# Kernel tuning notes

Hardware: AMD Instinct MI355X
Metric: run time of the kernel (lower is better)

The kernel has to match this reference:

```python
import jax, jax.numpy as jnp
import numpy as np

B, S, D, DOUT, E = 2, 2048, 1024, 1024, 8
DH = 4 * D  # expert hidden size


def setup_inputs() -> dict:
    key = jax.random.key(0)
    ks = jax.random.split(key, 7)
    sc = lambda *sh: 1.0 / np.sqrt(sh[-2]) if len(sh) >= 2 else 0.02
    return {
        "x": jax.random.normal(ks[0], (B, S, D), jnp.float32),
        "Wg": jax.random.normal(ks[1], (D, E), jnp.float32) / np.sqrt(D),
        "bg": jnp.zeros((E,), jnp.float32),
        "W1": jax.random.normal(ks[2], (E, D, DH), jnp.float32) / np.sqrt(D),
        "b1": jax.random.normal(ks[3], (E, DH), jnp.float32) * 0.02,
        "W2": jax.random.normal(ks[4], (E, DH, DOUT), jnp.float32) / np.sqrt(DH),
        "b2": jax.random.normal(ks[5], (E, DOUT), jnp.float32) * 0.02,
    }


def reference(x, Wg, bg, W1, b1, W2, b2):
    # x: [B, S, D] -> flatten tokens (chunking over seq in the original is
    # math-neutral: routing and expert MLP are per-token).
    Bb, Ss, Dd = x.shape
    xt = x.reshape(-1, Dd)                       # [T, D]
    # Gate: softmax then argmax (top-1 routing, output NOT scaled by gate prob)
    gates = jax.nn.softmax(xt @ Wg + bg, axis=-1)  # [T, E]
    sel = jnp.argmax(gates, axis=-1)               # [T]
    nE = W1.shape[0]
    out = jnp.zeros((xt.shape[0], W2.shape[-1]), x.dtype)
    # Grouped expert MLP expressed as masked dense loop over the small fixed
    # expert count (jit-friendly; a fused gather-grouped-GEMM-scatter kernel
    # is the optimization target).
    for e in range(nE):
        h = jax.nn.gelu(xt @ W1[e] + b1[e], approximate=False)  # [T, 4D]
        ye = h @ W2[e] + b2[e]                                  # [T, DOUT]
        out = jnp.where((sel == e)[:, None], ye, out)
    return out.reshape(Bb, Ss, -1)
```

## Files before the change

kernel.cpp:

```cpp
#include <hip/hip_runtime.h>
#include <hip/hip_bf16.h>
#include <math.h>

#define T_TOK 4096
#define DIM   1024
#define NEXP  8
#define DHID  4096
#define NDOUT 1024
#define BM    128
#define BN    128
#define BK    64
#define MAXTILES 40

typedef short bf16x8 __attribute__((ext_vector_type(8)));
typedef float f32x4 __attribute__((ext_vector_type(4)));

__device__ __forceinline__ unsigned short f2bf(float f) {
  unsigned u = __float_as_uint(f);
  u += 0x7fffu + ((u >> 16) & 1u);
  return (unsigned short)(u >> 16);
}
__device__ __forceinline__ unsigned pack2bf(float a, float b) {
  return (unsigned)f2bf(a) | ((unsigned)f2bf(b) << 16);
}
__device__ __forceinline__ int swz(int row, int kbyte) {
  return ((row << 7) + kbyte) ^ ((row & 7) << 4);
}

__global__ __launch_bounds__(256)
void gate_kernel(const float* __restrict__ x, const float* __restrict__ Wg,
                 const float* __restrict__ bg, int* __restrict__ sel) {
  int lane = threadIdx.x & 63;
  int wid  = threadIdx.x >> 6;
  int t = blockIdx.x * 4 + wid;
  if (t >= T_TOK) return;
  const float* xr = x + (size_t)t * DIM;
  double acc[NEXP];
#pragma unroll
  for (int e = 0; e < NEXP; e++) acc[e] = 0.0;
  for (int j = 0; j < DIM / 64; j++) {
    int d = lane + j * 64;
    float xv = xr[d];
    const float4* wr = reinterpret_cast<const float4*>(Wg + (size_t)d * NEXP);
    float4 w0 = wr[0], w1 = wr[1];
    acc[0] += (double)xv * (double)w0.x;
    acc[1] += (double)xv * (double)w0.y;
    acc[2] += (double)xv * (double)w0.z;
    acc[3] += (double)xv * (double)w0.w;
    acc[4] += (double)xv * (double)w1.x;
    acc[5] += (double)xv * (double)w1.y;
    acc[6] += (double)xv * (double)w1.z;
    acc[7] += (double)xv * (double)w1.w;
  }
#pragma unroll
  for (int off = 32; off >= 1; off >>= 1) {
#pragma unroll
    for (int e = 0; e < NEXP; e++) acc[e] += __shfl_down(acc[e], off);
  }
  if (lane == 0) {
    double best = acc[0] + (double)bg[0];
    int bi = 0;
#pragma unroll
    for (int e = 1; e < NEXP; e++) {
      double v = acc[e] + (double)bg[e];
      if (v > best) { best = v; bi = e; }
    }
    sel[t] = bi;
  }
}

__global__ void zero_kernel(int* __restrict__ counts) {
  if (threadIdx.x < NEXP) counts[threadIdx.x] = 0;
}

__global__ void hist_kernel(const int* __restrict__ sel, int* __restrict__ counts) {
  __shared__ int lc[NEXP];
  if (threadIdx.x < NEXP) lc[threadIdx.x] = 0;
  __syncthreads();
  int t = blockIdx.x * 256 + threadIdx.x;
  atomicAdd(&lc[sel[t]], 1);
  __syncthreads();
  if (threadIdx.x < NEXP) atomicAdd(&counts[threadIdx.x], lc[threadIdx.x]);
}

__global__ void plan_kernel(const int* __restrict__ counts, int* __restrict__ base,
                            int* __restrict__ cursor, int* __restrict__ tileExpert,
                            int* __restrict__ tilePos, int* __restrict__ tileRows,
                            int* __restrict__ ntiles) {
  if (threadIdx.x == 0) {
    int acc = 0, nt = 0;
    for (int e = 0; e < NEXP; e++) {
      base[e] = acc; cursor[e] = acc;
      int c = counts[e];
      for (int j = 0; j < c; j += BM) {
        tileExpert[nt] = e;
        tilePos[nt]    = acc + j;
        int rem = c - j;
        tileRows[nt]   = rem < BM ? rem : BM;
        nt++;
      }
      acc += c;
    }
    *ntiles = nt;
  }
}

__global__ void scatter_kernel(const int* __restrict__ sel, int* __restrict__ cursor,
                               int* __restrict__ list) {
  __shared__ int lcnt[NEXP];
  __shared__ int lbase[NEXP];
  int tid = threadIdx.x;
  if (tid < NEXP) lcnt[tid] = 0;
  __syncthreads();
  int t = blockIdx.x * 256 + tid;
  int e = sel[t];
  int lpos = atomicAdd(&lcnt[e], 1);
  __syncthreads();
  if (tid < NEXP) lbase[tid] = atomicAdd(&cursor[tid], lcnt[tid]);
  __syncthreads();
  list[lbase[e] + lpos] = t;
}

__global__ __launch_bounds__(256)
void gemm1_kernel(const float* __restrict__ x, const float* __restrict__ W1,
                  const float* __restrict__ b1, const int* __restrict__ list,
                  const int* __restrict__ tileExpert, const int* __restrict__ tilePos,
                  const int* __restrict__ tileRows, const int* __restrict__ ntiles,
                  unsigned short* __restrict__ Hc) {
  int tIdx = blockIdx.x;
  if (tIdx >= *ntiles) return;
  int e       = tileExpert[tIdx];
  int posBase = tilePos[tIdx];
  int rows    = tileRows[tIdx];
  int n0      = blockIdx.y * BN;

  __shared__ __align__(16) unsigned char AsB[BM * BK * 2];
  __shared__ __align__(16) unsigned char BsB[BN * BK * 2];

  const int tx   = threadIdx.x;
  const int lane = tx & 63;
  const int wid  = tx >> 6;
  const int wm = wid >> 1, wn = wid & 1;

  const int arow = tx >> 4;
  const int akq  = (tx & 15) << 2;
  int tok[8];
#pragma unroll
  for (int i = 0; i < 8; i++) {
    int r = arow + (i << 4);
    tok[i] = list[posBase + (r < rows ? r : 0)];
  }
  const int bn  = tx & 127;
  const int bk0 = (tx >> 7) << 2;
  const float* w1e = W1 + (size_t)e * DIM * DHID;

  f32x4 acc[4][4];
#pragma unroll
  for (int mf = 0; mf < 4; mf++)
#pragma unroll
    for (int nf = 0; nf < 4; nf++)
      acc[mf][nf] = f32x4{0.f, 0.f, 0.f, 0.f};

  for (int kt = 0; kt < DIM / BK; kt++) {
    int k0 = kt * BK;
#pragma unroll
    for (int i = 0; i < 8; i++) {
      int r = arow + (i << 4);
      float4 v = *reinterpret_cast<const float4*>(x + (size_t)tok[i] * DIM + (k0 + akq));
      uint2 p; p.x = pack2bf(v.x, v.y); p.y = pack2bf(v.z, v.w);
      *reinterpret_cast<uint2*>(AsB + swz(r, akq << 1)) = p;
    }
#pragma unroll
    for (int i = 0; i < 8; i++) {
      int kk = bk0 + (i << 3);
      const float* wp = w1e + (size_t)(k0 + kk) * DHID + (n0 + bn);
      float v0 = wp[0];
      float v1 = wp[DHID];
      float v2 = wp[2 * DHID];
      float v3 = wp[3 * DHID];
      uint2 p; p.x = pack2bf(v0, v1); p.y = pack2bf(v2, v3);
      *reinterpret_cast<uint2*>(BsB + swz(bn, kk << 1)) = p;
    }
    __syncthreads();
#pragma unroll
    for (int ks = 0; ks < 2; ks++) {
      int kbyte = ((ks << 5) + ((lane >> 4) << 3)) << 1;
      bf16x8 af[4], bfv[4];
#pragma unroll
      for (int mf = 0; mf < 4; mf++) {
        int row = (wm << 6) + (mf << 4) + (lane & 15);
        af[mf] = *reinterpret_cast<const bf16x8*>(AsB + swz(row, kbyte));
      }
#pragma unroll
      for (int nf = 0; nf < 4; nf++) {
        int col = (wn << 6) + (nf << 4) + (lane & 15);
        bfv[nf] = *reinterpret_cast<const bf16x8*>(BsB + swz(col, kbyte));
      }
#pragma unroll
      for (int mf = 0; mf < 4; mf++)
#pragma unroll
        for (int nf = 0; nf < 4; nf++)
          acc[mf][nf] = __builtin_amdgcn_mfma_f32_16x16x32_bf16(af[mf], bfv[nf], acc[mf][nf], 0, 0, 0);
    }
    __syncthreads();
  }

  const float* b1e = b1 + (size_t)e * DHID;
#pragma unroll
  for (int nf = 0; nf < 4; nf++) {
    int col = n0 + (wn << 6) + (nf << 4) + (lane & 15);
    float bias = b1e[col];
#pragma unroll
    for (int mf = 0; mf < 4; mf++) {
#pragma unroll
      for (int j = 0; j < 4; j++) {
        int rloc = (wm << 6) + (mf << 4) + ((lane >> 4) << 2) + j;
        if (rloc < rows) {
          float h = acc[mf][nf][j] + bias;
          float g = 0.5f * h * (1.0f + erff(h * 0.70710678118654752f));
          Hc[(size_t)(posBase + rloc) * DHID + col] = f2bf(g);
        }
      }
    }
  }
}

__global__ __launch_bounds__(256)
void gemm2_kernel(const unsigned short* __restrict__ Hc, const float* __restrict__ W2,
                  const float* __restrict__ b2, const int* __restrict__ list,
                  const int* __restrict__ tileExpert, const int* __restrict__ tilePos,
                  const int* __restrict__ tileRows, const int* __restrict__ ntiles,
                  float* __restrict__ out) {
  int tIdx = blockIdx.x;
  if (tIdx >= *ntiles) return;
  int e       = tileExpert[tIdx];
  int posBase = tilePos[tIdx];
  int rows    = tileRows[tIdx];
  int n0      = blockIdx.y * BN;

  __shared__ __align__(16) unsigned char AsB[BM * BK * 2];
  __shared__ __align__(16) unsigned char BsB[BN * BK * 2];

  const int tx   = threadIdx.x;
  const int lane = tx & 63;
  const int wid  = tx >> 6;
  const int wm = wid >> 1, wn = wid & 1;

  const int ar0 = tx >> 3;
  const int akq = (tx & 7) << 3;
  int arowIdx[4];
#pragma unroll
  for (int i = 0; i < 4; i++) {
    int r = ar0 + (i << 5);
    arowIdx[i] = posBase + (r < rows ? r : 0);
  }
  const int bn  = tx & 127;
  const int bk0 = (tx >> 7) << 2;
  const float* w2e = W2 + (size_t)e * DHID * NDOUT;

  f32x4 acc[4][4];
#pragma unroll
  for (int mf = 0; mf < 4; mf++)
#pragma unroll
    for (int nf = 0; nf < 4; nf++)
      acc[mf][nf] = f32x4{0.f, 0.f, 0.f, 0.f};

  for (int kt = 0; kt < DHID / BK; kt++) {
    int k0 = kt * BK;
#pragma unroll
    for (int i = 0; i < 4; i++) {
      int r = ar0 + (i << 5);
      int4 v = *reinterpret_cast<const int4*>(Hc + (size_t)arowIdx[i] * DHID + (k0 + akq));
      *reinterpret_cast<int4*>(AsB + swz(r, akq << 1)) = v;
    }
#pragma unroll
    for (int i = 0; i < 8; i++) {
      int kk = bk0 + (i << 3);
      const float* wp = w2e + (size_t)(k0 + kk) * NDOUT + (n0 + bn);
      float v0 = wp[0];
      float v1 = wp[NDOUT];
      float v2 = wp[2 * NDOUT];
      float v3 = wp[3 * NDOUT];
      uint2 p; p.x = pack2bf(v0, v1); p.y = pack2bf(v2, v3);
      *reinterpret_cast<uint2*>(BsB + swz(bn, kk << 1)) = p;
    }
    __syncthreads();
#pragma unroll
    for (int ks = 0; ks < 2; ks++) {
      int kbyte = ((ks << 5) + ((lane >> 4) << 3)) << 1;
      bf16x8 af[4], bfv[4];
#pragma unroll
      for (int mf = 0; mf < 4; mf++) {
        int row = (wm << 6) + (mf << 4) + (lane & 15);
        af[mf] = *reinterpret_cast<const bf16x8*>(AsB + swz(row, kbyte));
      }
#pragma unroll
      for (int nf = 0; nf < 4; nf++) {
        int col = (wn << 6) + (nf << 4) + (lane & 15);
        bfv[nf] = *reinterpret_cast<const bf16x8*>(BsB + swz(col, kbyte));
      }
#pragma unroll
      for (int mf = 0; mf < 4; mf++)
#pragma unroll
        for (int nf = 0; nf < 4; nf++)
          acc[mf][nf] = __builtin_amdgcn_mfma_f32_16x16x32_bf16(af[mf], bfv[nf], acc[mf][nf], 0, 0, 0);
    }
    __syncthreads();
  }

  const float* b2e = b2 + (size_t)e * NDOUT;
  int trow[4][4];
#pragma unroll
  for (int mf = 0; mf < 4; mf++)
#pragma unroll
    for (int j = 0; j < 4; j++) {
      int rloc = (wm << 6) + (mf << 4) + ((lane >> 4) << 2) + j;
      trow[mf][j] = (rloc < rows) ? list[posBase + rloc] : -1;
    }
#pragma unroll
  for (int nf = 0; nf < 4; nf++) {
    int col = n0 + (wn << 6) + (nf << 4) + (lane & 15);
    float bias = b2e[col];
#pragma unroll
    for (int mf = 0; mf < 4; mf++)
#pragma unroll
      for (int j = 0; j < 4; j++) {
        int t = trow[mf][j];
        if (t >= 0) out[(size_t)t * NDOUT + col] = acc[mf][nf][j] + bias;
      }
  }
}

extern "C" void kernel_launch(void* const* d_in, const int* in_sizes, int n_in,
                              void* d_out, int out_size, void* d_ws, size_t ws_size,
                              hipStream_t stream) {
  const float* x  = (const float*)d_in[0];
  const float* Wg = (const float*)d_in[1];
  const float* bg = (const float*)d_in[2];
  const float* W1 = (const float*)d_in[3];
  const float* b1 = (const float*)d_in[4];
  const float* W2 = (const float*)d_in[5];
  const float* b2 = (const float*)d_in[6];
  float* out = (float*)d_out;

  char* ws = (char*)d_ws;
  int* sel        = (int*)(ws);
  int* counts     = (int*)(ws + 16384);
  int* base       = (int*)(ws + 16448);
  int* cursor     = (int*)(ws + 16512);
  int* ntiles     = (int*)(ws + 16576);
  int* tileExpert = (int*)(ws + 16640);
  int* tilePos    = (int*)(ws + 16832);
  int* tileRows   = (int*)(ws + 17024);
  int* list       = (int*)(ws + 17408);
  unsigned short* Hc = (unsigned short*)(ws + 65536);

  gate_kernel<<<T_TOK / 4, 256, 0, stream>>>(x, Wg, bg, sel);
  zero_kernel<<<1, 64, 0, stream>>>(counts);
  hist_kernel<<<T_TOK / 256, 256, 0, stream>>>(sel, counts);
  plan_kernel<<<1, 64, 0, stream>>>(counts, base, cursor, tileExpert, tilePos, tileRows, ntiles);
  scatter_kernel<<<T_TOK / 256, 256, 0, stream>>>(sel, cursor, list);
  gemm1_kernel<<<dim3(MAXTILES, DHID / BN), 256, 0, stream>>>(
      x, W1, b1, list, tileExpert, tilePos, tileRows, ntiles, Hc);
  gemm2_kernel<<<dim3(MAXTILES, NDOUT / BN), 256, 0, stream>>>(
      Hc, W2, b2, list, tileExpert, tilePos, tileRows, ntiles, out);
}
```

Baseline: 344.8 us.

## Pre-convert weights to transposed bf16 and double-buffer GEMMs with direct global-to-LDS loads

Adds kernels that convert x to bf16 and transpose-convert W1/W2 into K-contiguous bf16 layouts each call. The grouped GEMMs then stage tiles with 16-byte global_load_lds into XOR-swizzled, double-buffered LDS, overlapping the next tile's load with MFMA compute. This removes per-element fp32 loads and conversions in the inner loop. The trade-off is an extra full pass over the weights each call and a large workspace.

```diff
diff --git a/kernel.cpp b/kernel.cpp
--- a/kernel.cpp
+++ b/kernel.cpp
@@ -23,8 +23,10 @@
 __device__ __forceinline__ unsigned pack2bf(float a, float b) {
   return (unsigned)f2bf(a) | ((unsigned)f2bf(b) << 16);
 }
-__device__ __forceinline__ int swz(int row, int kbyte) {
-  return ((row << 7) + kbyte) ^ ((row & 7) << 4);
+__device__ __forceinline__ void gl_lds16(const void* g, void* l) {
+  __builtin_amdgcn_global_load_lds(
+      (const __attribute__((address_space(1))) void*)g,
+      (__attribute__((address_space(3))) void*)l, 16, 0, 0);
 }
 
 __global__ __launch_bounds__(256)
@@ -122,7 +124,47 @@
 }
 
 __global__ __launch_bounds__(256)
-void gemm1_kernel(const float* __restrict__ x, const float* __restrict__ W1,
+void convert_x_kernel(const float* __restrict__ x, unsigned short* __restrict__ xbf) {
+  int i = (blockIdx.x * 256 + threadIdx.x) * 8;
+  float4 a = *(const float4*)(x + i);
+  float4 b = *(const float4*)(x + i + 4);
+  uint4 o;
+  o.x = pack2bf(a.x, a.y); o.y = pack2bf(a.z, a.w);
+  o.z = pack2bf(b.x, b.y); o.w = pack2bf(b.z, b.w);
+  *(uint4*)(xbf + i) = o;
+}
+
+__global__ __launch_bounds__(256)
+void transpose_convert_kernel(const float* __restrict__ in, unsigned short* __restrict__ out,
+                              int K, int N) {
+  int nb = blockIdx.x, kb = blockIdx.y, e = blockIdx.z;
+  const float* inp = in + (size_t)e * K * N;
+  unsigned short* outp = out + (size_t)e * N * K;
+  __shared__ unsigned short lds[64][72];
+  int tx = threadIdx.x;
+  int kloc = tx >> 4;
+  int n4   = (tx & 15) << 2;
+#pragma unroll
+  for (int p = 0; p < 4; p++) {
+    int k = p * 16 + kloc;
+    float4 v = *(const float4*)(inp + (size_t)(kb * 64 + k) * N + nb * 64 + n4);
+    lds[n4 + 0][k] = f2bf(v.x);
+    lds[n4 + 1][k] = f2bf(v.y);
+    lds[n4 + 2][k] = f2bf(v.z);
+    lds[n4 + 3][k] = f2bf(v.w);
+  }
+  __syncthreads();
+  int n  = tx >> 2;
+  int kq = (tx & 3) << 4;
+  uint4 a = *(const uint4*)&lds[n][kq];
+  uint4 b = *(const uint4*)&lds[n][kq + 8];
+  unsigned short* o = outp + (size_t)(nb * 64 + n) * K + kb * 64 + kq;
+  *(uint4*)o = a;
+  *(uint4*)(o + 8) = b;
+}
+
+__global__ __launch_bounds__(256)
+void gemm1_kernel(const unsigned short* __restrict__ xbf, const unsigned short* __restrict__ W1T,
                   const float* __restrict__ b1, const int* __restrict__ list,
                   const int* __restrict__ tileExpert, const int* __restrict__ tilePos,
                   const int* __restrict__ tileRows, const int* __restrict__ ntiles,
@@ -134,25 +176,26 @@
   int rows    = tileRows[tIdx];
   int n0      = blockIdx.y * BN;
 
-  __shared__ __align__(16) unsigned char AsB[BM * BK * 2];
-  __shared__ __align__(16) unsigned char BsB[BN * BK * 2];
+  __shared__ __align__(1024) unsigned char As[2][BM * 128];
+  __shared__ __align__(1024) unsigned char Bs[2][BN * 128];
 
   const int tx   = threadIdx.x;
   const int lane = tx & 63;
-  const int wid  = tx >> 6;
-  const int wm = wid >> 1, wn = wid & 1;
-
-  const int arow = tx >> 4;
-  const int akq  = (tx & 15) << 2;
-  int tok[8];
-#pragma unroll
-  for (int i = 0; i < 8; i++) {
-    int r = arow + (i << 4);
-    tok[i] = list[posBase + (r < rows ? r : 0)];
-  }
-  const int bn  = tx & 127;
-  const int bk0 = (tx >> 7) << 2;
-  const float* w1e = W1 + (size_t)e * DIM * DHID;
+  const int w    = tx >> 6;
+  const int wm = w >> 1, wn = w & 1;
+  const int u    = lane & 7;
+  const int rsub = lane >> 3;
+  const int px   = (u ^ rsub) << 4;
+
+  const char* aSrc[4];
+  const char* bSrc[4];
+#pragma unroll
+  for (int l = 0; l < 4; l++) {
+    int r = w * 32 + l * 8 + rsub;
+    int tok = list[posBase + (r < rows ? r : 0)];
+    aSrc[l] = (const char*)xbf + ((size_t)tok * DIM) * 2 + px;
+    bSrc[l] = (const char*)W1T + (((size_t)e * DHID + n0 + r) * DIM) * 2 + px;
+  }
 
   f32x4 acc[4][4];
 #pragma unroll
@@ -161,48 +204,46 @@
     for (int nf = 0; nf < 4; nf++)
       acc[mf][nf] = f32x4{0.f, 0.f, 0.f, 0.f};
 
-  for (int kt = 0; kt < DIM / BK; kt++) {
-    int k0 = kt * BK;
-#pragma unroll
-    for (int i = 0; i < 8; i++) {
-      int r = arow + (i << 4);
-      float4 v = *reinterpret_cast<const float4*>(x + (size_t)tok[i] * DIM + (k0 + akq));
-      uint2 p; p.x = pack2bf(v.x, v.y); p.y = pack2bf(v.z, v.w);
-      *reinterpret_cast<uint2*>(AsB + swz(r, akq << 1)) = p;
-    }
-#pragma unroll
-    for (int i = 0; i < 8; i++) {
-      int kk = bk0 + (i << 3);
-      const float* wp = w1e + (size_t)(k0 + kk) * DHID + (n0 + bn);
-      float v0 = wp[0];
-      float v1 = wp[DHID];
-      float v2 = wp[2 * DHID];
-      float v3 = wp[3 * DHID];
-      uint2 p; p.x = pack2bf(v0, v1); p.y = pack2bf(v2, v3);
-      *reinterpret_cast<uint2*>(BsB + swz(bn, kk << 1)) = p;
-    }
-    __syncthreads();
+  const int NT = DIM / BK;
+  auto stage = [&](int buf, int kt) {
+    int kb = kt * 128;
+#pragma unroll
+    for (int l = 0; l < 4; l++) {
+      gl_lds16(aSrc[l] + kb, &As[buf][(w * 32 + l * 8) * 128]);
+      gl_lds16(bSrc[l] + kb, &Bs[buf][(w * 32 + l * 8) * 128]);
+    }
+  };
+  auto compute = [&](int buf) {
 #pragma unroll
     for (int ks = 0; ks < 2; ks++) {
-      int kbyte = ((ks << 5) + ((lane >> 4) << 3)) << 1;
-      bf16x8 af[4], bfv[4];
+      int kbl = ks * 64 + (lane >> 4) * 16;
+      bf16x8 af[4], bv[4];
 #pragma unroll
       for (int mf = 0; mf < 4; mf++) {
         int row = (wm << 6) + (mf << 4) + (lane & 15);
-        af[mf] = *reinterpret_cast<const bf16x8*>(AsB + swz(row, kbyte));
+        af[mf] = *(const bf16x8*)&As[buf][row * 128 + (kbl ^ ((row & 7) << 4))];
       }
 #pragma unroll
       for (int nf = 0; nf < 4; nf++) {
-        int col = (wn << 6) + (nf << 4) + (lane & 15);
-        bfv[nf] = *reinterpret_cast<const bf16x8*>(BsB + swz(col, kbyte));
+        int row = (wn << 6) + (nf << 4) + (lane & 15);
+        bv[nf] = *(const bf16x8*)&Bs[buf][row * 128 + (kbl ^ ((row & 7) << 4))];
       }
 #pragma unroll
       for (int mf = 0; mf < 4; mf++)
 #pragma unroll
         for (int nf = 0; nf < 4; nf++)
-          acc[mf][nf] = __builtin_amdgcn_mfma_f32_16x16x32_bf16(af[mf], bfv[nf], acc[mf][nf], 0, 0, 0);
-    }
+          acc[mf][nf] = __builtin_amdgcn_mfma_f32_16x16x32_bf16(af[mf], bv[nf], acc[mf][nf], 0, 0, 0);
+    }
+  };
+
+  stage(0, 0);
+  __syncthreads();
+  int cur = 0;
+  for (int kt = 0; kt < NT; kt++) {
+    if (kt + 1 < NT) stage(cur ^ 1, kt + 1);
+    compute(cur);
     __syncthreads();
+    cur ^= 1;
   }
 
   const float* b1e = b1 + (size_t)e * DHID;
@@ -226,7 +267,7 @@
 }
 
 __global__ __launch_bounds__(256)
-void gemm2_kernel(const unsigned short* __restrict__ Hc, const float* __restrict__ W2,
+void gemm2_kernel(const unsigned short* __restrict__ Hc, const unsigned short* __restrict__ W2T,
                   const float* __restrict__ b2, const int* __restrict__ list,
                   const int* __restrict__ tileExpert, const int* __restrict__ tilePos,
                   const int* __restrict__ tileRows, const int* __restrict__ ntiles,
@@ -238,25 +279,26 @@
   int rows    = tileRows[tIdx];
   int n0      = blockIdx.y * BN;
 
-  __shared__ __align__(16) unsigned char AsB[BM * BK * 2];
-  __shared__ __align__(16) unsigned char BsB[BN * BK * 2];
+  __shared__ __align__(1024) unsigned char As[2][BM * 128];
+  __shared__ __align__(1024) unsigned char Bs[2][BN * 128];
 
   const int tx   = threadIdx.x;
   const int lane = tx & 63;
-  const int wid  = tx >> 6;
-  const int wm = wid >> 1, wn = wid & 1;
-
-  const int ar0 = tx >> 3;
-  const int akq = (tx & 7) << 3;
-  int arowIdx[4];
-#pragma unroll
-  for (int i = 0; i < 4; i++) {
-    int r = ar0 + (i << 5);
-    arowIdx[i] = posBase + (r < rows ? r : 0);
-  }
-  const int bn  = tx & 127;
-  const int bk0 = (tx >> 7) << 2;
-  const float* w2e = W2 + (size_t)e * DHID * NDOUT;
+  const int w    = tx >> 6;
+  const int wm = w >> 1, wn = w & 1;
+  const int u    = lane & 7;
+  const int rsub = lane >> 3;
+  const int px   = (u ^ rsub) << 4;
+
+  const char* aSrc[4];
+  const char* bSrc[4];
+#pragma unroll
+  for (int l = 0; l < 4; l++) {
+    int r = w * 32 + l * 8 + rsub;
+    int ar = posBase + (r < rows ? r : 0);
+    aSrc[l] = (const char*)Hc + ((size_t)ar * DHID) * 2 + px;
+    bSrc[l] = (const char*)W2T + (((size_t)e * NDOUT + n0 + r) * DHID) * 2 + px;
+  }
 
   f32x4 acc[4][4];
 #pragma unroll
@@ -265,47 +307,46 @@
     for (int nf = 0; nf < 4; nf++)
       acc[mf][nf] = f32x4{0.f, 0.f, 0.f, 0.f};
 
-  for (int kt = 0; kt < DHID / BK; kt++) {
-    int k0 = kt * BK;
-#pragma unroll
-    for (int i = 0; i < 4; i++) {
-      int r = ar0 + (i << 5);
-      int4 v = *reinterpret_cast<const int4*>(Hc + (size_t)arowIdx[i] * DHID + (k0 + akq));
-      *reinterpret_cast<int4*>(AsB + swz(r, akq << 1)) = v;
-    }
-#pragma unroll
-    for (int i = 0; i < 8; i++) {
-      int kk = bk0 + (i << 3);
-      const float* wp = w2e + (size_t)(k0 + kk) * NDOUT + (n0 + bn);
-      float v0 = wp[0];
-      float v1 = wp[NDOUT];
-      float v2 = wp[2 * NDOUT];
-      float v3 = wp[3 * NDOUT];
-      uint2 p; p.x = pack2bf(v0, v1); p.y = pack2bf(v2, v3);
-      *reinterpret_cast<uint2*>(BsB + swz(bn, kk << 1)) = p;
-    }
-    __syncthreads();
+  const int NT = DHID / BK;
+  auto stage = [&](int buf, int kt) {
+    int kb = kt * 128;
+#pragma unroll
+    for (int l = 0; l < 4; l++) {
+      gl_lds16(aSrc[l] + kb, &As[buf][(w * 32 + l * 8) * 128]);
+      gl_lds16(bSrc[l] + kb, &Bs[buf][(w * 32 + l * 8) * 128]);
+    }
+  };
+  auto compute = [&](int buf) {
 #pragma unroll
     for (int ks = 0; ks < 2; ks++) {
-      int kbyte = ((ks << 5) + ((lane >> 4) << 3)) << 1;
-      bf16x8 af[4], bfv[4];
+      int kbl = ks * 64 + (lane >> 4) * 16;
+      bf16x8 af[4], bv[4];
 #pragma unroll
       for (int mf = 0; mf < 4; mf++) {
         int row = (wm << 6) + (mf << 4) + (lane & 15);
-        af[mf] = *reinterpret_cast<const bf16x8*>(AsB + swz(row, kbyte));
+        af[mf] = *(const bf16x8*)&As[buf][row * 128 + (kbl ^ ((row & 7) << 4))];
       }
 #pragma unroll
       for (int nf = 0; nf < 4; nf++) {
-        int col = (wn << 6) + (nf << 4) + (lane & 15);
-        bfv[nf] = *reinterpret_cast<const bf16x8*>(BsB + swz(col, kbyte));
+        int row = (wn << 6) + (nf << 4) + (lane & 15);
+        bv[nf] = *(const bf16x8*)&Bs[buf][row * 128 + (kbl ^ ((row & 7) << 4))];
       }
 #pragma unroll
       for (int mf = 0; mf < 4; mf++)
 #pragma unroll
         for (int nf = 0; nf < 4; nf++)
-          acc[mf][nf] = __builtin_amdgcn_mfma_f32_16x16x32_bf16(af[mf], bfv[nf], acc[mf][nf], 0, 0, 0);
-    }
+          acc[mf][nf] = __builtin_amdgcn_mfma_f32_16x16x32_bf16(af[mf], bv[nf], acc[mf][nf], 0, 0, 0);
+    }
+  };
+
+  stage(0, 0);
+  __syncthreads();
+  int cur = 0;
+  for (int kt = 0; kt < NT; kt++) {
+    if (kt + 1 < NT) stage(cur ^ 1, kt + 1);
+    compute(cur);
     __syncthreads();
+    cur ^= 1;
   }
 
   const float* b2e = b2 + (size_t)e * NDOUT;
@@ -353,15 +394,24 @@
   int* tilePos    = (int*)(ws + 16832);
   int* tileRows   = (int*)(ws + 17024);
   int* list       = (int*)(ws + 17408);
-  unsigned short* Hc = (unsigned short*)(ws + 65536);
+
+  unsigned short* xbf = (unsigned short*)(ws + (1ull << 20));
+  unsigned short* Hc  = (unsigned short*)(ws + (16ull << 20));
+  unsigned short* W1T = (unsigned short*)(ws + (48ull << 20));
+  unsigned short* W2T = (unsigned short*)(ws + (112ull << 20));
 
   gate_kernel<<<T_TOK / 4, 256, 0, stream>>>(x, Wg, bg, sel);
   zero_kernel<<<1, 64, 0, stream>>>(counts);
   hist_kernel<<<T_TOK / 256, 256, 0, stream>>>(sel, counts);
   plan_kernel<<<1, 64, 0, stream>>>(counts, base, cursor, tileExpert, tilePos, tileRows, ntiles);
   scatter_kernel<<<T_TOK / 256, 256, 0, stream>>>(sel, cursor, list);
+
+  convert_x_kernel<<<T_TOK * DIM / (256 * 8), 256, 0, stream>>>(x, xbf);
+  transpose_convert_kernel<<<dim3(DHID / 64, DIM / 64, NEXP), 256, 0, stream>>>(W1, W1T, DIM, DHID);
+  transpose_convert_kernel<<<dim3(NDOUT / 64, DHID / 64, NEXP), 256, 0, stream>>>(W2, W2T, DHID, NDOUT);
+
   gemm1_kernel<<<dim3(MAXTILES, DHID / BN), 256, 0, stream>>>(
-      x, W1, b1, list, tileExpert, tilePos, tileRows, ntiles, Hc);
+      xbf, W1T, b1, list, tileExpert, tilePos, tileRows, ntiles, Hc);
   gemm2_kernel<<<dim3(MAXTILES, NDOUT / BN), 256, 0, stream>>>(
-      Hc, W2, b2, list, tileExpert, tilePos, tileRows, ntiles, out);
-}
+      Hc, W2T, b2, list, tileExpert, tilePos, tileRows, ntiles, out);
+}
```

Result: faster. 320.5 us (-7.1%).
